# Kernel tuning notes

Measured on AMD Instinct MI355X. Metric: run time of the kernel, lower is better.

## Reference

```python
import jax, jax.numpy as jnp
import numpy as np

B, N, C = 4, 1370, 1024
H, DH = 16, C // 16
N_ROPE = 1369  # patch tokens covered by RoPE (prefix=1 CLS token)


def _rotate_half(x):
    x1, x2 = jnp.split(x, 2, axis=-1)
    return jnp.concatenate([-x2, x1], axis=-1)


def _rope_apply(x, sin, cos):
    return x * cos + _rotate_half(x) * sin


def setup_inputs() -> dict:
    key = jax.random.key(0)
    ks = jax.random.split(key, 7)
    return {
        "x": jax.random.normal(ks[0], (B, N, C), dtype=jnp.float32),
        "sin": jax.random.normal(ks[1], (N_ROPE, DH), dtype=jnp.float32),
        "cos": jax.random.normal(ks[2], (N_ROPE, DH), dtype=jnp.float32),
        "w_qkv": jax.random.normal(ks[3], (C, 3 * C), dtype=jnp.float32) * (C ** -0.5),
        "b_qkv": jax.random.normal(ks[4], (3 * C,), dtype=jnp.float32) * 0.02,
        "w_proj": jax.random.normal(ks[5], (C, C), dtype=jnp.float32) * (C ** -0.5),
        "b_proj": jax.random.normal(ks[6], (C,), dtype=jnp.float32) * 0.02,
    }


def reference(x, sin, cos, w_qkv, b_qkv, w_proj, b_proj):
    b, n, c = x.shape
    # QKV projection -> [3, B, H, N, DH]
    qkv = (x @ w_qkv + b_qkv).reshape(b, n, 3, H, DH).transpose(2, 0, 3, 1, 4)
    q, k, v = qkv[0], qkv[1], qkv[2]
    # RoPE on the last N_ROPE tokens (prefix tokens, e.g. CLS, left untouched)
    prefix = n - sin.shape[-2]
    q = jnp.concatenate([q[:, :, :prefix, :], _rope_apply(q[:, :, prefix:, :], sin, cos)], axis=-2)
    k = jnp.concatenate([k[:, :, :prefix, :], _rope_apply(k[:, :, prefix:, :], sin, cos)], axis=-2)
    # Full attention
    scale = 1.0 / jnp.sqrt(jnp.asarray(DH, dtype=x.dtype))
    attn = jnp.einsum('bhqd,bhkd->bhqk', q, k) * scale
    attn = jax.nn.softmax(attn, axis=-1)
    out = jnp.einsum('bhqk,bhkd->bhqd', attn, v)
    out = out.transpose(0, 2, 1, 3).reshape(b, n, c)
    return out @ w_proj + b_proj
```

## Files before the change

kernel.cpp:

```cpp
#include <hip/hip_runtime.h>
#include <hip/hip_bf16.h>

#define B_ 4
#define N_ 1370
#define C_ 1024
#define H_ 16
#define DH_ 64
#define NR_ 1369
#define M_ (B_*N_)
#define VTS_ 1408
#define ALS 64
#define PLS 72

#define QSCALE 0.1803368801111f

typedef _Float16 f16x8  __attribute__((ext_vector_type(8)));
typedef __bf16   bf16x8 __attribute__((ext_vector_type(8)));
typedef float    f32x4  __attribute__((ext_vector_type(4)));

__device__ __forceinline__ f16x8 ld_frag_h(const unsigned short* p) {
    uint4 u = *(const uint4*)p;
    return __builtin_bit_cast(f16x8, u);
}
__device__ __forceinline__ bf16x8 ld_frag_b(const unsigned short* p) {
    uint4 u = *(const uint4*)p;
    return __builtin_bit_cast(bf16x8, u);
}
__device__ __forceinline__ unsigned short f2h(float f) {
    _Float16 h = (_Float16)f;
    return __builtin_bit_cast(unsigned short, h);
}
__device__ __forceinline__ unsigned short f2bf(float f) {
    __hip_bfloat16 h = __float2bfloat16(f);
    return __builtin_bit_cast(unsigned short, h);
}
__device__ __forceinline__ bf16x8 ones_bf() {
    uint4 u = make_uint4(0x3F803F80u, 0x3F803F80u, 0x3F803F80u, 0x3F803F80u);
    return __builtin_bit_cast(bf16x8, u);
}

__device__ __forceinline__ void load_lds16(const unsigned short* g, unsigned short* l) {
    __builtin_amdgcn_global_load_lds(
        (const __attribute__((address_space(1))) unsigned int*)g,
        (__attribute__((address_space(3))) unsigned int*)l,
        16, 0, 0);
}

__global__ __launch_bounds__(256)
void conv_x_k(const float* __restrict__ x, unsigned short* __restrict__ xo, int total4) {
    int i = blockIdx.x * 256 + threadIdx.x;
    if (i >= total4) return;
    float4 v = ((const float4*)x)[i];
    ushort4 h;
    h.x = f2h(v.x); h.y = f2h(v.y); h.z = f2h(v.z); h.w = f2h(v.w);
    ((ushort4*)xo)[i] = h;
}

__global__ __launch_bounds__(256)
void conv_wt_k(const float* __restrict__ w, unsigned short* __restrict__ wt, int Ncol) {
    __shared__ unsigned short Th[64][68];
    const int tid = threadIdx.x, tx = tid & 15, ty = tid >> 4;
    const int k0 = blockIdx.y * 64, n0 = blockIdx.x * 64;
    #pragma unroll
    for (int i = 0; i < 4; ++i) {
        const int k = ty + i * 16;
        float4 v = *(const float4*)&w[(size_t)(k0 + k) * Ncol + n0 + tx * 4];
        Th[k][tx*4+0] = f2h(v.x); Th[k][tx*4+1] = f2h(v.y);
        Th[k][tx*4+2] = f2h(v.z); Th[k][tx*4+3] = f2h(v.w);
    }
    __syncthreads();
    #pragma unroll
    for (int i = 0; i < 4; ++i) {
        const int n = ty + i * 16;
        ushort4 o;
        o.x = Th[tx*4+0][n]; o.y = Th[tx*4+1][n]; o.z = Th[tx*4+2][n]; o.w = Th[tx*4+3][n];
        *(ushort4*)&wt[(size_t)(n0 + n) * 1024 + k0 + tx * 4] = o;
    }
}

__global__ __launch_bounds__(256)
void transpose_v_k(const unsigned short* __restrict__ v, unsigned short* __restrict__ vt) {
    __shared__ unsigned short Th[64][68];
    const int tid = threadIdx.x, tx = tid & 15, ty = tid >> 4;
    const int bh = blockIdx.y, t0 = blockIdx.x * 64;
    const unsigned short* vp = v + (size_t)bh * N_ * DH_;
    unsigned short* vtp = vt + (size_t)bh * DH_ * VTS_;
    #pragma unroll
    for (int i = 0; i < 4; ++i) {
        const int tok = ty + i * 16;
        const int gtok = t0 + tok;
        ushort4 val;
        if (gtok < N_) val = *(const ushort4*)&vp[(size_t)gtok * DH_ + tx * 4];
        else { val.x = 0; val.y = 0; val.z = 0; val.w = 0; }
        Th[tok][tx*4+0] = val.x; Th[tok][tx*4+1] = val.y;
        Th[tok][tx*4+2] = val.z; Th[tok][tx*4+3] = val.w;
    }
    __syncthreads();
    #pragma unroll
    for (int i = 0; i < 4; ++i) {
        const int d = ty + i * 16;
        ushort4 o;
        o.x = Th[tx*4+0][d]; o.y = Th[tx*4+1][d]; o.z = Th[tx*4+2][d]; o.w = Th[tx*4+3][d];
        *(ushort4*)&vtp[(size_t)d * VTS_ + t0 + tx * 4] = o;
    }
}

__global__ __launch_bounds__(512, 4)
void gemm_qkv8(const unsigned short* __restrict__ A, const unsigned short* __restrict__ Bt,
               const float* __restrict__ bias,
               unsigned short* __restrict__ qb, unsigned short* __restrict__ kb,
               unsigned short* __restrict__ vb,
               const float* __restrict__ sinp, const float* __restrict__ cosp)
{
    __shared__ __align__(16) unsigned short A_s[2][192 * 64];
    __shared__ __align__(16) unsigned short B_s[2][128 * 64];

    const int tid = threadIdx.x;
    const int wave = tid >> 6, lane = tid & 63;
    const int quad = lane >> 4, l16 = lane & 15;
    const int m0 = blockIdx.y * 192, n0 = blockIdx.x * 128;
    const int mwave = (wave >> 1) * 48;
    const int nwave = (wave & 1) * 64;

    const int srow = lane >> 3;
    const int gseg = (lane & 7) ^ srow;

    f32x4 acc[3][4] = {};

    auto stage = [&](int kc, int buf) {
        const int kof = kc * 64;
        #pragma unroll
        for (int i = 0; i < 3; ++i) {
            const int rbase = wave * 24 + i * 8;
            int arow = m0 + rbase + srow;
            if (arow > M_ - 1) arow = M_ - 1;
            load_lds16(A + (size_t)arow * 1024 + kof + gseg * 8, &A_s[buf][rbase * 64]);
        }
        #pragma unroll
        for (int i = 0; i < 2; ++i) {
            const int rbase = wave * 16 + i * 8;
            const int brow = n0 + rbase + srow;
            load_lds16(Bt + (size_t)brow * 1024 + kof + gseg * 8, &B_s[buf][rbase * 64]);
        }
    };

    stage(0, 0);

    for (int kc = 0; kc < 16; ++kc) {
        const int cur = kc & 1;
        __syncthreads();
        if (kc + 1 < 16) stage(kc + 1, cur ^ 1);

        #pragma unroll
        for (int kh = 0; kh < 2; ++kh) {
            const int soff = (((kh * 4 + quad) ^ (l16 & 7)) << 3);
            f16x8 a[3], b[4];
            #pragma unroll
            for (int t = 0; t < 3; ++t)
                a[t] = ld_frag_h(&A_s[cur][(mwave + t * 16 + l16) * 64 + soff]);
            #pragma unroll
            for (int t = 0; t < 4; ++t)
                b[t] = ld_frag_h(&B_s[cur][(nwave + t * 16 + l16) * 64 + soff]);
            #pragma unroll
            for (int i = 0; i < 3; ++i)
                #pragma unroll
                for (int j = 0; j < 4; ++j)
                    acc[i][j] = __builtin_amdgcn_mfma_f32_16x16x32_f16(a[i], b[j], acc[i][j], 0, 0, 0);
        }
    }

    const int nbase = n0 + nwave;
    const int part = nbase >> 10;
    const int h = (nbase & 1023) >> 6;
    #pragma unroll
    for (int i = 0; i < 3; ++i) {
        #pragma unroll
        for (int r = 0; r < 4; ++r) {
            const int gm = m0 + mwave + i * 16 + quad * 4 + r;
            if (gm >= M_) continue;
            const int b = gm / N_;
            const int tok = gm - b * N_;

            float val[4];
            #pragma unroll
            for (int j = 0; j < 4; ++j)
                val[j] = acc[i][j][r] + bias[nbase + j * 16 + l16];

            if (part < 2 && tok >= 1) {
                const float* sp = sinp + (size_t)(tok - 1) * DH_;
                const float* cp = cosp + (size_t)(tok - 1) * DH_;
                const float s0 = sp[l16],      s1 = sp[16 + l16];
                const float s2 = sp[32 + l16], s3 = sp[48 + l16];
                const float c0 = cp[l16],      c1 = cp[16 + l16];
                const float c2 = cp[32 + l16], c3 = cp[48 + l16];
                const float n0v = fmaf(val[0], c0, -val[2] * s0);
                const float n1v = fmaf(val[1], c1, -val[3] * s1);
                const float n2v = fmaf(val[2], c2,  val[0] * s2);
                const float n3v = fmaf(val[3], c3,  val[1] * s3);
                val[0] = n0v; val[1] = n1v; val[2] = n2v; val[3] = n3v;
            }

            const int bh = b * H_ + h;
            #pragma unroll
            for (int j = 0; j < 4; ++j) {
                const int d = j * 16 + l16;
                if (part == 0)      qb[((size_t)bh * N_ + tok) * DH_ + d] = f2h(val[j] * QSCALE);
                else if (part == 1) kb[((size_t)bh * N_ + tok) * DH_ + d] = f2h(val[j]);
                else                vb[((size_t)bh * N_ + tok) * DH_ + d] = f2bf(val[j]);
            }
        }
    }
}

template<int MT>
__global__ __launch_bounds__(256)
void gemm_mfma(const unsigned short* __restrict__ A, const unsigned short* __restrict__ Bt,
               const float* __restrict__ bias, float* __restrict__ out, int nchunks)
{
    constexpr int MI = MT / 32;
    __shared__ __align__(16) unsigned short A_s[MT * 64];
    __shared__ __align__(16) unsigned short B_s[128 * 64];

    const int tid = threadIdx.x;
    const int wave = tid >> 6, lane = tid & 63;
    const int quad = lane >> 4, l16 = lane & 15;
    const int m0 = blockIdx.y * MT, n0 = blockIdx.x * 128;
    const int mwave = (wave & 1) * (MT / 2), nwave = (wave >> 1) * 64;

    const int srow = lane >> 3;
    const int gseg = (lane & 7) ^ srow;

    f32x4 acc[MI][4] = {};

    for (int kc = 0; kc < nchunks; ++kc) {
        const int kof = kc * 64;

        __syncthreads();
        #pragma unroll
        for (int i = 0; i < MI; ++i) {
            const int rbase = wave * (8 * MI) + i * 8;
            int arow = m0 + rbase + srow;
            if (arow > M_ - 1) arow = M_ - 1;
            load_lds16(A + (size_t)arow * 1024 + kof + gseg * 8, &A_s[rbase * 64]);
        }
        #pragma unroll
        for (int i = 0; i < 4; ++i) {
            const int rbase = wave * 32 + i * 8;
            const int brow = n0 + rbase + srow;
            load_lds16(Bt + (size_t)brow * 1024 + kof + gseg * 8, &B_s[rbase * 64]);
        }
        __syncthreads();

        #pragma unroll
        for (int kh = 0; kh < 2; ++kh) {
            const int soff = (((kh * 4 + quad) ^ (l16 & 7)) << 3);
            f16x8 a[MI], b[4];
            #pragma unroll
            for (int t = 0; t < MI; ++t)
                a[t] = ld_frag_h(&A_s[(mwave + t * 16 + l16) * 64 + soff]);
            #pragma unroll
            for (int t = 0; t < 4; ++t)
                b[t] = ld_frag_h(&B_s[(nwave + t * 16 + l16) * 64 + soff]);
            #pragma unroll
            for (int i = 0; i < MI; ++i)
                #pragma unroll
                for (int j = 0; j < 4; ++j)
                    acc[i][j] = __builtin_amdgcn_mfma_f32_16x16x32_f16(a[i], b[j], acc[i][j], 0, 0, 0);
        }
    }

    #pragma unroll
    for (int i = 0; i < MI; ++i) {
        #pragma unroll
        for (int r = 0; r < 4; ++r) {
            const int gm = m0 + mwave + i * 16 + quad * 4 + r;
            if (gm >= M_) continue;
            #pragma unroll
            for (int j = 0; j < 4; ++j) {
                const int gn = n0 + nwave + j * 16 + l16;
                out[(size_t)gm * 1024 + gn] = acc[i][j][r] + bias[gn];
            }
        }
    }
}

__global__ __launch_bounds__(256)
void attn_k(const unsigned short* __restrict__ q, const unsigned short* __restrict__ k,
            const unsigned short* __restrict__ vt, unsigned short* __restrict__ out)
{
    __shared__ __align__(16) unsigned short Ks[2][64 * ALS];
    __shared__ __align__(16) unsigned short Vs[2][64 * ALS];
    __shared__ __align__(16) unsigned short Ps[4 * 32 * PLS];

    const int tid  = threadIdx.x;
    const int wave = tid >> 6, lane = tid & 63;
    const int quad = lane >> 4, l16 = lane & 15;
    const int srow = lane >> 3;
    const int gseg = (lane & 7) ^ srow;
    const int bh = blockIdx.y;
    const int q0 = blockIdx.x * 128;

    const unsigned short* qp  = q  + (size_t)bh * N_ * DH_;
    const unsigned short* kp  = k  + (size_t)bh * N_ * DH_;
    const unsigned short* vtp = vt + (size_t)bh * DH_ * VTS_;

    f16x8 qf[2][2];
    #pragma unroll
    for (int s = 0; s < 2; ++s) {
        int qrow = q0 + wave * 32 + s * 16 + l16;
        if (qrow > N_ - 1) qrow = N_ - 1;
        qf[s][0] = ld_frag_h(qp + (size_t)qrow * DH_ + quad * 8);
        qf[s][1] = ld_frag_h(qp + (size_t)qrow * DH_ + 32 + quad * 8);
    }

    const bf16x8 onesv = ones_bf();
    f32x4 O[2][4] = {};
    f32x4 L[2] = {};

    unsigned short* Pw = Ps + wave * 32 * PLS;
    const int so0 = ((quad)     ^ (l16 & 7)) << 3;
    const int so1 = ((4 + quad) ^ (l16 & 7)) << 3;

    auto stage = [&](int ch, int buf) {
        const int k0 = ch * 64;
        #pragma unroll
        for (int i = 0; i < 2; ++i) {
            const int rbase = wave * 16 + i * 8;
            int krow = k0 + rbase + srow;
            if (krow > N_ - 1) krow = N_ - 1;
            load_lds16(kp + (size_t)krow * DH_ + gseg * 8, &Ks[buf][rbase * ALS]);
            load_lds16(vtp + (size_t)(rbase + srow) * VTS_ + k0 + gseg * 8, &Vs[buf][rbase * ALS]);
        }
    };

    stage(0, 0);

    for (int ch = 0; ch < 22; ++ch) {
        const int k0 = ch * 64;
        const int cur = ch & 1;
        __syncthreads();
        if (ch + 1 < 22) stage(ch + 1, 1 - cur);

        f16x8 kf[4][2];
        #pragma unroll
        for (int t = 0; t < 4; ++t) {
            kf[t][0] = ld_frag_h(&Ks[cur][(t * 16 + l16) * ALS + so0]);
            kf[t][1] = ld_frag_h(&Ks[cur][(t * 16 + l16) * ALS + so1]);
        }
        f32x4 S[2][4];
        __builtin_amdgcn_s_setprio(1);
        #pragma unroll
        for (int s = 0; s < 2; ++s) {
            #pragma unroll
            for (int t = 0; t < 4; ++t) {
                f32x4 z = {};
                z = __builtin_amdgcn_mfma_f32_16x16x32_f16(qf[s][0], kf[t][0], z, 0, 0, 0);
                z = __builtin_amdgcn_mfma_f32_16x16x32_f16(qf[s][1], kf[t][1], z, 0, 0, 0);
                S[s][t] = z;
            }
        }
        __builtin_amdgcn_s_setprio(0);
        if (k0 + 64 > N_) {
            #pragma unroll
            for (int t = 0; t < 4; ++t) {
                if (k0 + t * 16 + l16 >= N_) {
                    #pragma unroll
                    for (int s = 0; s < 2; ++s) {
                        S[s][t][0] = -1e30f; S[s][t][1] = -1e30f;
                        S[s][t][2] = -1e30f; S[s][t][3] = -1e30f;
                    }
                }
            }
        }

        #pragma unroll
        for (int s = 0; s < 2; ++s) {
            #pragma unroll
            for (int t = 0; t < 4; ++t) {
                #pragma unroll
                for (int r = 0; r < 4; ++r) {
                    const float p = __builtin_amdgcn_exp2f(S[s][t][r]);
                    Pw[(s * 16 + quad * 4 + r) * PLS + t * 16 + l16] = f2bf(p);
                }
            }
        }
        __builtin_amdgcn_wave_barrier();

        bf16x8 pf[2][2];
        #pragma unroll
        for (int s = 0; s < 2; ++s) {
            pf[s][0] = ld_frag_b(&Pw[(s * 16 + l16) * PLS + quad * 8]);
            pf[s][1] = ld_frag_b(&Pw[(s * 16 + l16) * PLS + 32 + quad * 8]);
        }
        bf16x8 vf[4][2];
        #pragma unroll
        for (int dt = 0; dt < 4; ++dt) {
            vf[dt][0] = ld_frag_b(&Vs[cur][(dt * 16 + l16) * ALS + so0]);
            vf[dt][1] = ld_frag_b(&Vs[cur][(dt * 16 + l16) * ALS + so1]);
        }
        __builtin_amdgcn_s_setprio(1);
        #pragma unroll
        for (int s = 0; s < 2; ++s) {
            L[s] = __builtin_amdgcn_mfma_f32_16x16x32_bf16(pf[s][0], onesv, L[s], 0, 0, 0);
            L[s] = __builtin_amdgcn_mfma_f32_16x16x32_bf16(pf[s][1], onesv, L[s], 0, 0, 0);
            #pragma unroll
            for (int dt = 0; dt < 4; ++dt) {
                O[s][dt] = __builtin_amdgcn_mfma_f32_16x16x32_bf16(pf[s][0], vf[dt][0], O[s][dt], 0, 0, 0);
                O[s][dt] = __builtin_amdgcn_mfma_f32_16x16x32_bf16(pf[s][1], vf[dt][1], O[s][dt], 0, 0, 0);
            }
        }
        __builtin_amdgcn_s_setprio(0);
    }

    const int b = bh >> 4, h = bh & 15;
    #pragma unroll
    for (int s = 0; s < 2; ++s) {
        #pragma unroll
        for (int r = 0; r < 4; ++r) {
            const int qi = q0 + wave * 32 + s * 16 + quad * 4 + r;
            if (qi < N_) {
                const float inv = 1.0f / L[s][r];
                unsigned short* op = out + ((size_t)(b * N_ + qi)) * C_ + h * DH_ + l16;
                #pragma unroll
                for (int dt = 0; dt < 4; ++dt) op[dt * 16] = f2h(O[s][dt][r] * inv);
            }
        }
    }
}

extern "C" void kernel_launch(void* const* d_in, const int* in_sizes, int n_in,
                              void* d_out, int out_size, void* d_ws, size_t ws_size,
                              hipStream_t stream) {
    const float* x      = (const float*)d_in[0];
    const float* sinp   = (const float*)d_in[1];
    const float* cosp   = (const float*)d_in[2];
    const float* w_qkv  = (const float*)d_in[3];
    const float* b_qkv  = (const float*)d_in[4];
    const float* w_proj = (const float*)d_in[5];
    const float* b_proj = (const float*)d_in[6];
    float* out = (float*)d_out;

    unsigned short* p = (unsigned short*)d_ws;
    const size_t xsz  = (size_t)M_ * C_;
    const size_t wqsz = (size_t)3 * C_ * C_;
    const size_t wpsz = (size_t)C_ * C_;
    const size_t hsz  = (size_t)B_ * H_ * N_ * DH_;
    const size_t vtsz = (size_t)B_ * H_ * DH_ * VTS_;
    unsigned short* x_h   = p;            p += xsz;
    unsigned short* wq_t  = p;            p += wqsz;
    unsigned short* wp_t  = p;            p += wpsz;
    unsigned short* q     = p;            p += hsz;
    unsigned short* k     = p;            p += hsz;
    unsigned short* vt    = p;            p += vtsz;
    unsigned short* attnb = p;            p += xsz;
    unsigned short* vb    = attnb;

    conv_x_k<<<(int)((xsz / 4 + 255) / 256), 256, 0, stream>>>(x, x_h, (int)(xsz / 4));
    conv_wt_k<<<dim3(3 * C_ / 64, C_ / 64), 256, 0, stream>>>(w_qkv, wq_t, 3 * C_);
    conv_wt_k<<<dim3(C_ / 64, C_ / 64), 256, 0, stream>>>(w_proj, wp_t, C_);

    gemm_qkv8<<<dim3(3 * C_ / 128, (M_ + 191) / 192), 512, 0, stream>>>(
        x_h, wq_t, b_qkv, q, k, vb, sinp, cosp);

    transpose_v_k<<<dim3(VTS_ / 64, B_ * H_), 256, 0, stream>>>(vb, vt);

    attn_k<<<dim3((N_ + 127) / 128, B_ * H_), 256, 0, stream>>>(q, k, vt, attnb);

    gemm_mfma<64><<<dim3(C_ / 128, (M_ + 63) / 64), 256, 0, stream>>>(
        attnb, wp_t, b_proj, out, 16);
}
```

Measured before the change: 255.0 us.

## Split attention work across eight waves and remap blocks for XCD locality

The attention kernel moves from 4 waves handling 32 query rows each to 8 waves handling 16 rows each, keeping the 128-row query tile per block. K/V staging is split across more waves, so each wave issues one load pair instead of two. The grid is flattened to 1D, and block ids are remapped so that consecutive heads land on the same XCD, which should improve L2 reuse of K/V. The setprio hints are dropped and launch bounds now request higher occupancy; each wave reuses loaded K/V fragments over fewer query rows, which costs more LDS reads per unit of MFMA work.

```diff
diff --git a/kernel.cpp b/kernel.cpp
--- a/kernel.cpp
+++ b/kernel.cpp
@@ -284,53 +284,52 @@
     }
 }
 
-__global__ __launch_bounds__(256)
+__global__ __launch_bounds__(512, 6)
 void attn_k(const unsigned short* __restrict__ q, const unsigned short* __restrict__ k,
             const unsigned short* __restrict__ vt, unsigned short* __restrict__ out)
 {
     __shared__ __align__(16) unsigned short Ks[2][64 * ALS];
     __shared__ __align__(16) unsigned short Vs[2][64 * ALS];
-    __shared__ __align__(16) unsigned short Ps[4 * 32 * PLS];
+    __shared__ __align__(16) unsigned short Ps[8 * 16 * PLS];
 
     const int tid  = threadIdx.x;
     const int wave = tid >> 6, lane = tid & 63;
     const int quad = lane >> 4, l16 = lane & 15;
     const int srow = lane >> 3;
     const int gseg = (lane & 7) ^ srow;
-    const int bh = blockIdx.y;
-    const int q0 = blockIdx.x * 128;
+
+    const int id  = blockIdx.x;
+    const int lid = (id & 7) * 88 + (id >> 3);
+    const int bh  = lid / 11;
+    const int q0  = (lid - bh * 11) * 128;
 
     const unsigned short* qp  = q  + (size_t)bh * N_ * DH_;
     const unsigned short* kp  = k  + (size_t)bh * N_ * DH_;
     const unsigned short* vtp = vt + (size_t)bh * DH_ * VTS_;
 
-    f16x8 qf[2][2];
-    #pragma unroll
-    for (int s = 0; s < 2; ++s) {
-        int qrow = q0 + wave * 32 + s * 16 + l16;
+    f16x8 qf[2];
+    {
+        int qrow = q0 + wave * 16 + l16;
         if (qrow > N_ - 1) qrow = N_ - 1;
-        qf[s][0] = ld_frag_h(qp + (size_t)qrow * DH_ + quad * 8);
-        qf[s][1] = ld_frag_h(qp + (size_t)qrow * DH_ + 32 + quad * 8);
+        qf[0] = ld_frag_h(qp + (size_t)qrow * DH_ + quad * 8);
+        qf[1] = ld_frag_h(qp + (size_t)qrow * DH_ + 32 + quad * 8);
     }
 
     const bf16x8 onesv = ones_bf();
-    f32x4 O[2][4] = {};
-    f32x4 L[2] = {};
-
-    unsigned short* Pw = Ps + wave * 32 * PLS;
+    f32x4 O[4] = {};
+    f32x4 L = {};
+
+    unsigned short* Pw = Ps + wave * 16 * PLS;
     const int so0 = ((quad)     ^ (l16 & 7)) << 3;
     const int so1 = ((4 + quad) ^ (l16 & 7)) << 3;
 
     auto stage = [&](int ch, int buf) {
         const int k0 = ch * 64;
-        #pragma unroll
-        for (int i = 0; i < 2; ++i) {
-            const int rbase = wave * 16 + i * 8;
-            int krow = k0 + rbase + srow;
-            if (krow > N_ - 1) krow = N_ - 1;
-            load_lds16(kp + (size_t)krow * DH_ + gseg * 8, &Ks[buf][rbase * ALS]);
-            load_lds16(vtp + (size_t)(rbase + srow) * VTS_ + k0 + gseg * 8, &Vs[buf][rbase * ALS]);
-        }
+        const int rbase = wave * 8;
+        int krow = k0 + rbase + srow;
+        if (krow > N_ - 1) krow = N_ - 1;
+        load_lds16(kp + (size_t)krow * DH_ + gseg * 8, &Ks[buf][rbase * ALS]);
+        load_lds16(vtp + (size_t)(rbase + srow) * VTS_ + k0 + gseg * 8, &Vs[buf][rbase * ALS]);
     };
 
     stage(0, 0);
@@ -347,83 +346,62 @@
             kf[t][0] = ld_frag_h(&Ks[cur][(t * 16 + l16) * ALS + so0]);
             kf[t][1] = ld_frag_h(&Ks[cur][(t * 16 + l16) * ALS + so1]);
         }
-        f32x4 S[2][4];
-        __builtin_amdgcn_s_setprio(1);
-        #pragma unroll
-        for (int s = 0; s < 2; ++s) {
-            #pragma unroll
-            for (int t = 0; t < 4; ++t) {
-                f32x4 z = {};
-                z = __builtin_amdgcn_mfma_f32_16x16x32_f16(qf[s][0], kf[t][0], z, 0, 0, 0);
-                z = __builtin_amdgcn_mfma_f32_16x16x32_f16(qf[s][1], kf[t][1], z, 0, 0, 0);
-                S[s][t] = z;
-            }
-        }
-        __builtin_amdgcn_s_setprio(0);
+        f32x4 S[4];
+        #pragma unroll
+        for (int t = 0; t < 4; ++t) {
+            f32x4 z = {};
+            z = __builtin_amdgcn_mfma_f32_16x16x32_f16(qf[0], kf[t][0], z, 0, 0, 0);
+            z = __builtin_amdgcn_mfma_f32_16x16x32_f16(qf[1], kf[t][1], z, 0, 0, 0);
+            S[t] = z;
+        }
         if (k0 + 64 > N_) {
             #pragma unroll
             for (int t = 0; t < 4; ++t) {
                 if (k0 + t * 16 + l16 >= N_) {
-                    #pragma unroll
-                    for (int s = 0; s < 2; ++s) {
-                        S[s][t][0] = -1e30f; S[s][t][1] = -1e30f;
-                        S[s][t][2] = -1e30f; S[s][t][3] = -1e30f;
-                    }
+                    S[t][0] = -1e30f; S[t][1] = -1e30f;
+                    S[t][2] = -1e30f; S[t][3] = -1e30f;
                 }
             }
         }
 
         #pragma unroll
-        for (int s = 0; s < 2; ++s) {
-            #pragma unroll
-            for (int t = 0; t < 4; ++t) {
-                #pragma unroll
-                for (int r = 0; r < 4; ++r) {
-                    const float p = __builtin_amdgcn_exp2f(S[s][t][r]);
-                    Pw[(s * 16 + quad * 4 + r) * PLS + t * 16 + l16] = f2bf(p);
-                }
+        for (int t = 0; t < 4; ++t) {
+            #pragma unroll
+            for (int r = 0; r < 4; ++r) {
+                const float p = __builtin_amdgcn_exp2f(S[t][r]);
+                Pw[(quad * 4 + r) * PLS + t * 16 + l16] = f2bf(p);
             }
         }
         __builtin_amdgcn_wave_barrier();
 
-        bf16x8 pf[2][2];
-        #pragma unroll
-        for (int s = 0; s < 2; ++s) {
-            pf[s][0] = ld_frag_b(&Pw[(s * 16 + l16) * PLS + quad * 8]);
-            pf[s][1] = ld_frag_b(&Pw[(s * 16 + l16) * PLS + 32 + quad * 8]);
-        }
+        bf16x8 pf[2];
+        pf[0] = ld_frag_b(&Pw[l16 * PLS + quad * 8]);
+        pf[1] = ld_frag_b(&Pw[l16 * PLS + 32 + quad * 8]);
+
         bf16x8 vf[4][2];
         #pragma unroll
         for (int dt = 0; dt < 4; ++dt) {
             vf[dt][0] = ld_frag_b(&Vs[cur][(dt * 16 + l16) * ALS + so0]);
             vf[dt][1] = ld_frag_b(&Vs[cur][(dt * 16 + l16) * ALS + so1]);
         }
-        __builtin_amdgcn_s_setprio(1);
-        #pragma unroll
-        for (int s = 0; s < 2; ++s) {
-            L[s] = __builtin_amdgcn_mfma_f32_16x16x32_bf16(pf[s][0], onesv, L[s], 0, 0, 0);
-            L[s] = __builtin_amdgcn_mfma_f32_16x16x32_bf16(pf[s][1], onesv, L[s], 0, 0, 0);
-            #pragma unroll
-            for (int dt = 0; dt < 4; ++dt) {
-                O[s][dt] = __builtin_amdgcn_mfma_f32_16x16x32_bf16(pf[s][0], vf[dt][0], O[s][dt], 0, 0, 0);
-                O[s][dt] = __builtin_amdgcn_mfma_f32_16x16x32_bf16(pf[s][1], vf[dt][1], O[s][dt], 0, 0, 0);
-            }
-        }
-        __builtin_amdgcn_s_setprio(0);
+        L = __builtin_amdgcn_mfma_f32_16x16x32_bf16(pf[0], onesv, L, 0, 0, 0);
+        L = __builtin_amdgcn_mfma_f32_16x16x32_bf16(pf[1], onesv, L, 0, 0, 0);
+        #pragma unroll
+        for (int dt = 0; dt < 4; ++dt) {
+            O[dt] = __builtin_amdgcn_mfma_f32_16x16x32_bf16(pf[0], vf[dt][0], O[dt], 0, 0, 0);
+            O[dt] = __builtin_amdgcn_mfma_f32_16x16x32_bf16(pf[1], vf[dt][1], O[dt], 0, 0, 0);
+        }
     }
 
     const int b = bh >> 4, h = bh & 15;
     #pragma unroll
-    for (int s = 0; s < 2; ++s) {
-        #pragma unroll
-        for (int r = 0; r < 4; ++r) {
-            const int qi = q0 + wave * 32 + s * 16 + quad * 4 + r;
-            if (qi < N_) {
-                const float inv = 1.0f / L[s][r];
-                unsigned short* op = out + ((size_t)(b * N_ + qi)) * C_ + h * DH_ + l16;
-                #pragma unroll
-                for (int dt = 0; dt < 4; ++dt) op[dt * 16] = f2h(O[s][dt][r] * inv);
-            }
+    for (int r = 0; r < 4; ++r) {
+        const int qi = q0 + wave * 16 + quad * 4 + r;
+        if (qi < N_) {
+            const float inv = 1.0f / L[r];
+            unsigned short* op = out + ((size_t)(b * N_ + qi)) * C_ + h * DH_ + l16;
+            #pragma unroll
+            for (int dt = 0; dt < 4; ++dt) op[dt * 16] = f2h(O[dt][r] * inv);
         }
     }
 }
@@ -464,7 +442,7 @@
 
     transpose_v_k<<<dim3(VTS_ / 64, B_ * H_), 256, 0, stream>>>(vb, vt);
 
-    attn_k<<<dim3((N_ + 127) / 128, B_ * H_), 256, 0, stream>>>(q, k, vt, attnb);
+    attn_k<<<dim3(11 * B_ * H_), 512, 0, stream>>>(q, k, vt, attnb);
 
     gemm_mfma<64><<<dim3(C_ / 128, (M_ + 63) / 64), 256, 0, stream>>>(
         attnb, wp_t, b_proj, out, 16);
```

New measurement: 235.0 us. 7.9% less time.
